# Performance work log

Hardware: AMD Instinct MI355X
Metric: run time of the kernel (lower is better)

The kernel has to match this reference:

```python
import jax, jax.numpy as jnp
import numpy as np
import math

N, E, D, H = 50000, 1600000, 128, 8
DH = D // H  # per-head dim
EPS = 1e-5   # batchnorm eps


def _attn(q_in, k_in, v_in, Wq, Wk, Wv, src, dst):
    # GAT-style edge attention: score = exp(clip(<K[src],Q[dst]>/sqrt(DH), -5, 5))
    Q = (q_in @ Wq.T).reshape(-1, H, DH)
    K = (k_in @ Wk.T).reshape(-1, H, DH)
    V = (v_in @ Wv.T).reshape(-1, H, DH)
    score = jnp.exp(jnp.clip((K[src] * Q[dst]).sum(-1) / math.sqrt(DH), -5.0, 5.0))  # [E,H]
    wV = jax.ops.segment_sum(V[src] * score[:, :, None], dst, num_segments=N)  # [N,H,DH]
    z = jax.ops.segment_sum(score, dst, num_segments=N)                         # [N,H]
    return (wV / z[:, :, None]).reshape(-1, D)


def _bn(x, gamma, beta):
    # BatchNorm1d in training mode: biased batch stats over nodes
    m = x.mean(0)
    v = x.var(0)
    return (x - m) / jnp.sqrt(v + EPS) * gamma + beta


def setup_inputs() -> dict:
    key = jax.random.key(0)
    ks = iter(jax.random.split(key, 48))

    def w(shape, scale=None):
        s = scale if scale is not None else 1.0 / math.sqrt(shape[-1])
        return jax.random.normal(next(ks), shape, jnp.float32) * s

    inp = dict(
        h=w((N, D), 1.0),
        sv=w((N, D), 1.0),
        src=jax.random.randint(next(ks), (E,), 0, N, jnp.int32),
        dst=jax.random.randint(next(ks), (E,), 0, N, jnp.int32),
    )
    for nm in ["Wq_sv", "Wk_sv", "Wv_sv", "Wq_cv", "Wk_cv", "Wv_cv",
               "Wq_sh", "Wk_sh", "Wv_sh"]:
        inp[nm] = w((D, D))
    inp.update(
        Wo=w((D, 2 * D)), bo=jnp.zeros((D,), jnp.float32),
        Wo_h=w((D, 2 * D)), bo_h=jnp.zeros((D,), jnp.float32),
        W1=w((2 * D, D)), b1=jnp.zeros((2 * D,), jnp.float32),
        W2=w((D, 2 * D)), b2=jnp.zeros((D,), jnp.float32),
        W1h=w((2 * D, D)), b1h=jnp.zeros((2 * D,), jnp.float32),
        W2h=w((D, 2 * D)), b2h=jnp.zeros((D,), jnp.float32),
        Wg1=w((D, D)), bg1=jnp.zeros((D,), jnp.float32),
        Wg2=w((D, D)), bg2=jnp.zeros((D,), jnp.float32),
        gbn1=jnp.ones((D,), jnp.float32), bbn1=jnp.zeros((D,), jnp.float32),
        gbn2=jnp.ones((D,), jnp.float32), bbn2=jnp.zeros((D,), jnp.float32),
        gbn1h=jnp.ones((D,), jnp.float32), bbn1h=jnp.zeros((D,), jnp.float32),
        gbn2h=jnp.ones((D,), jnp.float32), bbn2h=jnp.zeros((D,), jnp.float32),
    )
    return inp


def reference(h, sv, src, dst,
              Wq_sv, Wk_sv, Wv_sv, Wq_cv, Wk_cv, Wv_cv, Wq_sh, Wk_sh, Wv_sh,
              Wo, bo, Wo_h, bo_h,
              W1, b1, W2, b2, W1h, b1h, W2h, b2h,
              Wg1, bg1, Wg2, bg2,
              gbn1, bbn1, gbn2, bbn2, gbn1h, bbn1h, gbn2h, bbn2h):
    h_in1, sv_in1 = h, sv
    # --- h branch ---
    a_self = _attn(h, h, h, Wq_sv, Wk_sv, Wv_sv, src, dst)
    a_cross = _attn(h, sv, sv, Wq_cv, Wk_cv, Wv_cv, src, dst)
    hO = jnp.concatenate([a_self, a_cross], -1) @ Wo.T + bo
    h1 = _bn(h_in1 + hO, gbn1, bbn1)
    ffn = jax.nn.relu(h1 @ W1.T + b1) @ W2.T + b2
    h_out = _bn(h1 + ffn, gbn2, bbn2)
    # --- state-vector branch ---
    a_self_h = _attn(sv, sv, sv, Wq_sh, Wk_sh, Wv_sh, src, dst)
    # faithful to source: cross_attention_v weights reused here
    a_cross_h = _attn(sv, h_in1, h_in1, Wq_cv, Wk_cv, Wv_cv, src, dst)
    svO = jnp.concatenate([a_self_h, a_cross_h], -1) @ Wo_h.T + bo_h
    g1 = jax.nn.sigmoid(h_in1 @ Wg1.T + bg1)
    sv1 = _bn((1.0 - g1) * sv_in1 + g1 * svO, gbn1h, bbn1h)
    ffn_h = jax.nn.relu(sv1 @ W1h.T + b1h) @ W2h.T + b2h
    g2 = jax.nn.sigmoid(h_in1 @ Wg2.T + bg2)
    sv_out = _bn((1.0 - g2) * sv1 + g2 * ffn_h, gbn2h, bbn2h)
    return (h_out, sv_out)
```

## Files before the change

### kernel.cpp

```cpp
#include <hip/hip_runtime.h>

typedef _Float16 f16x8 __attribute__((ext_vector_type(8)));
typedef _Float16 f16x2 __attribute__((ext_vector_type(2)));
typedef __fp16 fp16x2_raw __attribute__((ext_vector_type(2)));
typedef float f32x4 __attribute__((ext_vector_type(4)));
typedef float f32x2 __attribute__((ext_vector_type(2)));
typedef unsigned int uint32;
typedef unsigned short ushort16;
typedef unsigned char uchar;

#define EPS_BN 1e-5f

__device__ __forceinline__ uint32 pk16(float a, float b){
  fp16x2_raw h = __builtin_amdgcn_cvt_pkrtz(a, b);
  return *(uint32*)&h;
}
__device__ __forceinline__ uchar f2fp8(float f){
  uint32 p = __builtin_amdgcn_cvt_pk_fp8_f32(f, f, 0, false);
  return (uchar)(p & 0xff);
}
__device__ __forceinline__ f32x2 fp8pair_lo(uint32 w){
  return __builtin_amdgcn_cvt_pk_f32_fp8(w, false);
}
__device__ __forceinline__ f32x2 fp8pair_hi(uint32 w){
  return __builtin_amdgcn_cvt_pk_f32_fp8(w, true);
}

struct WEnt { const float* s; const float* s2; ushort16* d; int KD, MD, nfrag; };
struct WConv { WEnt e[16]; };

__global__ __launch_bounds__(256) void prep_k(WConv wc,
    const float* __restrict__ a, const float* __restrict__ b,
    ushort16* __restrict__ da, ushort16* __restrict__ db, int n,
    const int* __restrict__ dst, int* __restrict__ bcnt, int E, int shift){
  int y = blockIdx.y;
  if (y < 2){
    const float* s = y ? b : a;
    ushort16* d = y ? db : da;
    int i = (blockIdx.x * 256 + threadIdx.x) * 4;
    if (i >= n) return;
    float4 v = *(const float4*)(s + i);
    uint2 p;
    p.x = pk16(v.x, v.y);
    p.y = pk16(v.z, v.w);
    *(uint2*)(d + i) = p;
  } else if (y == 2){
    __shared__ int lh[128];
    if (blockIdx.x >= 512) return;
    int tid = threadIdx.x;
    if (tid < 128) lh[tid] = 0;
    __syncthreads();
    int stride = 512 * 256;
    for (int i = blockIdx.x * 256 + tid; i < E; i += stride)
      atomicAdd(&lh[dst[i] >> shift], 1);
    __syncthreads();
    if (tid < 128 && lh[tid]) atomicAdd(&bcnt[tid], lh[tid]);
  } else {
    if (blockIdx.x >= 256) return;
    WEnt t = wc.e[blockIdx.x >> 4];
    int fid = (blockIdx.x & 15) * 256 + threadIdx.x;
    if (fid >= t.nfrag) return;
    int lane = fid & 63, sm = fid >> 6;
    int MT = t.MD >> 4;
    int s = sm / MT, m = sm - s * MT;
    int row = m * 16 + (lane & 15);
    int col = s * 32 + (lane >> 4) * 8;
    const float* sp = t.s;
    if (t.s2 && row >= 128){ sp = t.s2; row -= 128; }
    const float* p = sp + (size_t)row * t.KD + col;
    uint4 o;
    o.x = pk16(p[0], p[1]); o.y = pk16(p[2], p[3]);
    o.z = pk16(p[4], p[5]); o.w = pk16(p[6], p[7]);
    *(uint4*)(t.d + (size_t)fid * 8) = o;
  }
}

__global__ __launch_bounds__(64) void bscan_k(const int* __restrict__ bcnt,
    int* __restrict__ bstart, int* __restrict__ bcur, int B){
  if (threadIdx.x == 0){
    int run = 0;
    for (int b = 0; b < B; b++){ bstart[b] = run; bcur[b] = run; run += bcnt[b]; }
    bstart[B] = run;
  }
}

#define BIN_TB 512
#define BIN_TILE 4096
__global__ __launch_bounds__(512) void bin_k(const int* __restrict__ src, const int* __restrict__ dst,
                                             int* __restrict__ bcur, uint2* __restrict__ ebuf,
                                             int E, int shift, int B){
  __shared__ int lhist[128];
  __shared__ int lstart[128];
  __shared__ int gbase[128];
  __shared__ uint2 lpair[BIN_TILE];
  int tid = threadIdx.x;
  int base = blockIdx.x * BIN_TILE;
  int cnt = E - base; if (cnt > BIN_TILE) cnt = BIN_TILE;
  if (tid < 128) lhist[tid] = 0;
  __syncthreads();
  int myb[8], myrank[8];
  uint2 myp[8];
  int nmine = 0;
  #pragma unroll
  for (int j = 0; j < 8; j++){
    int i = tid + j * BIN_TB;
    if (i < cnt){
      int s = src[base + i], d = dst[base + i];
      int b = d >> shift;
      myp[nmine] = make_uint2((uint32)s, (uint32)d);
      myb[nmine] = b;
      myrank[nmine] = atomicAdd(&lhist[b], 1);
      nmine++;
    }
  }
  __syncthreads();
  if (tid == 0){
    int run = 0;
    for (int b = 0; b < B; b++){ lstart[b] = run; run += lhist[b]; }
  }
  __syncthreads();
  if (tid < B) gbase[tid] = atomicAdd(&bcur[tid], lhist[tid]);
  for (int j = 0; j < nmine; j++){
    lpair[lstart[myb[j]] + myrank[j]] = myp[j];
  }
  __syncthreads();
  for (int i = tid; i < cnt; i += BIN_TB){
    uint2 p = lpair[i];
    int b = (int)(p.y >> shift);
    ebuf[gbase[b] + (i - lstart[b])] = p;
  }
}

#define CSR_TB 1024
__global__ __launch_bounds__(1024) void csr_k(const uint2* __restrict__ ebuf,
    const int* __restrict__ bstart, int* __restrict__ row_off, int* __restrict__ esrc,
    int shift, int N, int E, int B){
  __shared__ int lc[4096];
  __shared__ int lcur[4096];
  __shared__ int wsum[16];
  int b = blockIdx.x;
  int d0 = b << shift;
  int nd = 1 << shift; if (d0 + nd > N) nd = N - d0;
  if (nd <= 0) return;
  int e0 = bstart[b], e1 = bstart[b + 1];
  int tid = threadIdx.x, lane = tid & 63, wv = tid >> 6;
  for (int j = tid; j < nd; j += CSR_TB){ lc[j] = 0; lcur[j] = 0; }
  __syncthreads();
  for (int i = e0 + tid; i < e1; i += CSR_TB){
    atomicAdd(&lc[(int)ebuf[i].y - d0], 1);
  }
  __syncthreads();
  int base4 = tid * 4;
  int v0 = (base4 + 0 < nd) ? lc[base4 + 0] : 0;
  int v1 = (base4 + 1 < nd) ? lc[base4 + 1] : 0;
  int v2 = (base4 + 2 < nd) ? lc[base4 + 2] : 0;
  int v3 = (base4 + 3 < nd) ? lc[base4 + 3] : 0;
  int ts = v0 + v1 + v2 + v3;
  int inc = ts;
  #pragma unroll
  for (int d = 1; d < 64; d <<= 1){
    int t = __shfl_up(inc, d);
    if (lane >= d) inc += t;
  }
  if (lane == 63) wsum[wv] = inc;
  __syncthreads();
  int woff = 0;
  for (int w = 0; w < 16; w++) if (w < wv) woff += wsum[w];
  int excl = woff + (inc - ts);
  int o0 = excl, o1 = o0 + v0, o2 = o1 + v1, o3 = o2 + v2;
  __syncthreads();
  if (base4 + 0 < nd){ lc[base4 + 0] = o0; row_off[d0 + base4 + 0] = e0 + o0; }
  if (base4 + 1 < nd){ lc[base4 + 1] = o1; row_off[d0 + base4 + 1] = e0 + o1; }
  if (base4 + 2 < nd){ lc[base4 + 2] = o2; row_off[d0 + base4 + 2] = e0 + o2; }
  if (base4 + 3 < nd){ lc[base4 + 3] = o3; row_off[d0 + base4 + 3] = e0 + o3; }
  __syncthreads();
  for (int i = e0 + tid; i < e1; i += CSR_TB){
    uint2 p = ebuf[i];
    int d = (int)p.y - d0;
    int r = atomicAdd(&lcur[d], 1);
    esrc[e0 + lc[d] + r] = (int)p.x;
  }
  if (b == B - 1 && tid == 0) row_off[N] = E;
}

template<int KD, int MD, int EPI, int ABN, int ST, int GS>
__device__ __forceinline__ void gemm_body(
    const ushort16* __restrict__ X, const ushort16* __restrict__ W,
    const float* __restrict__ bias, const float* __restrict__ bias2,
    const ushort16* __restrict__ resb, const ushort16* __restrict__ gatep,
    const float* __restrict__ rstats, const float* __restrict__ rg, const float* __restrict__ rb,
    const float* __restrict__ astats, const float* __restrict__ ag, const float* __restrict__ ab,
    ushort16* __restrict__ outb, float* __restrict__ stats_out, int N, float invN,
    _Float16* OsBase, float* sstB, float* sst2B)
{
  constexpr int KS = KD / 32;
  constexpr int MT = MD / 16;
  constexpr int LSTR = MD + 8;
  int lane = threadIdx.x & 63, wv = threadIdx.x >> 6;
  _Float16* OsW = OsBase + wv * 16 * LSTR;
  int l15 = lane & 15, kq = lane >> 4;
  int rowbase = (blockIdx.x * 4 + wv) * 16;
  int row = rowbase + l15;
  int rc = row < N ? row : N - 1;
  const f16x8* ap = (const f16x8*)(X + (size_t)rc * KD + kq * 8);
  f16x8 a[KS];
  #pragma unroll
  for (int s = 0; s < KS; s++) a[s] = ap[s * 4];
  if constexpr (ABN){
    #pragma unroll
    for (int s = 0; s < KS; s++){
      #pragma unroll
      for (int j = 0; j < 8; j++){
        int c = s * 32 + kq * 8 + j;
        float mm = astats[c] * invN;
        float var = astats[128 + c] * invN - mm * mm;
        float rs = rsqrtf(var + EPS_BN);
        float scc = rs * ag[c];
        float shh = ab[c] - mm * scc;
        a[s][j] = (_Float16)((float)a[s][j] * scc + shh);
      }
    }
  }
  const f16x8* Wf = (const f16x8*)W;
  f32x4 acc[MT];
  #pragma unroll
  for (int m = 0; m < MT; m++) acc[m] = (f32x4)(0.f);
  #pragma unroll
  for (int s = 0; s < KS; s++){
    #pragma unroll
    for (int m = 0; m < MT; m++){
      acc[m] = __builtin_amdgcn_mfma_f32_16x16x32_f16(a[s], Wf[(s * MT + m) * 64 + lane], acc[m], 0, 0, 0);
    }
  }
  float ps[MT], ps2[MT];
  if constexpr (ST){
    #pragma unroll
    for (int m = 0; m < MT; m++){ ps[m] = 0.f; ps2[m] = 0.f; }
  }
  int r0 = rowbase + kq * 4;
  #pragma unroll
  for (int m = 0; m < MT; m++){
    int col = m * 16 + l15;
    float bv;
    if (bias2 && col >= 128) bv = bias2[col - 128];
    else bv = bias[col];
    float sc = 0.f, sh = 0.f;
    if constexpr (EPI == 5 || EPI == 6){
      float mm = rstats[col] * invN;
      float var = rstats[128 + col] * invN - mm * mm;
      float rs = rsqrtf(var + EPS_BN);
      sc = rs * rg[col]; sh = rb[col] - mm * sc;
    }
    #pragma unroll
    for (int r = 0; r < 4; r++){
      int rr = r0 + r;
      float v;
      {
        int rrc = rr < N ? rr : N - 1;
        v = acc[m][r] + bv;
        if constexpr (EPI == 1) v = fmaxf(v, 0.f);
        if constexpr (EPI == 2) v = 1.f / (1.f + __expf(-v));
        if constexpr (EPI == 3){
          union { ushort16 u; _Float16 h; } cv; cv.u = resb[(size_t)rrc * 128 + col];
          v += (float)cv.h;
        }
        if constexpr (EPI == 5){
          union { ushort16 u; _Float16 h; } cv; cv.u = resb[(size_t)rrc * 128 + col];
          v += (float)cv.h * sc + sh;
        }
        if constexpr (EPI == 4 || EPI == 6){
          union { ushort16 u; _Float16 h; } gv; gv.u = gatep[(size_t)rrc * GS + col];
          union { ushort16 u; _Float16 h; } cv; cv.u = resb[(size_t)rrc * 128 + col];
          float g = (float)gv.h;
          float rv = (float)cv.h;
          if constexpr (EPI == 6) rv = rv * sc + sh;
          v = (1.f - g) * rv + g * v;
        }
      }
      OsW[(kq * 4 + r) * LSTR + col] = (_Float16)v;
      if constexpr (ST){
        if (rr < N){ ps[m] += v; ps2[m] += v * v; }
      }
    }
  }
  if constexpr (MD == 128){
    #pragma unroll
    for (int p = 0; p < 4; p++){
      int lrow = p * 4 + (lane >> 4);
      int rr = rowbase + lrow;
      int col8 = l15 * 8;
      if (rr < N){
        uint4 ov = *(uint4*)&OsW[lrow * LSTR + col8];
        *(uint4*)(outb + (size_t)rr * MD + col8) = ov;
      }
    }
  } else {
    #pragma unroll
    for (int p = 0; p < 8; p++){
      int lrow = p * 2 + (lane >> 5);
      int rr = rowbase + lrow;
      int col8 = (lane & 31) * 8;
      if (rr < N){
        uint4 ov = *(uint4*)&OsW[lrow * LSTR + col8];
        *(uint4*)(outb + (size_t)rr * MD + col8) = ov;
      }
    }
  }
  if constexpr (ST){
    #pragma unroll
    for (int m = 0; m < MT; m++){
      float s = ps[m], s2 = ps2[m];
      s  += __shfl_xor(s, 16);  s  += __shfl_xor(s, 32);
      s2 += __shfl_xor(s2, 16); s2 += __shfl_xor(s2, 32);
      if (lane < 16){ sstB[wv * 128 + m * 16 + l15] = s; sst2B[wv * 128 + m * 16 + l15] = s2; }
    }
    __syncthreads();
    int tid = threadIdx.x;
    if (tid < 128){
      atomicAdd(&stats_out[tid], sstB[tid] + sstB[128 + tid] + sstB[256 + tid] + sstB[384 + tid]);
    } else {
      int c = tid - 128;
      atomicAdd(&stats_out[tid], sst2B[c] + sst2B[128 + c] + sst2B[256 + c] + sst2B[384 + c]);
    }
  }
}

struct QkvArgs {
  const ushort16* Xq[4];
  const ushort16* Xkv[4];
  const ushort16* Wq[4];
  const ushort16* Wk[4];
  const ushort16* Wv[4];
  ushort16* Qo[4];
};
__global__ __launch_bounds__(256) void qkvg_k(
    QkvArgs A, uchar* __restrict__ KV8,
    const ushort16* __restrict__ Xg, const ushort16* __restrict__ Wg,
    const float* __restrict__ bg1, const float* __restrict__ bg2,
    ushort16* __restrict__ Gout, int N, float invN)
{
  __shared__ char smem[38144];
  int slot = blockIdx.y;
  if (slot == 4){
    _Float16* Os = (_Float16*)smem;
    float* sst  = (float*)(smem + 33792);
    float* sst2 = (float*)(smem + 33792 + 2048);
    gemm_body<128,256,2,0,0,256>(Xg, Wg, bg1, bg2, nullptr, nullptr,
        nullptr, nullptr, nullptr, nullptr, nullptr, nullptr,
        Gout, nullptr, N, invN, Os, sst, sst2);
    return;
  }
  _Float16* Qs = (_Float16*)smem;
  uchar* Ks = (uchar*)(smem + 17408);
  uchar* Vs = (uchar*)(smem + 17408 + 8704);
  int toff = slot << 8;
  const ushort16* Xq = A.Xq[slot];
  const ushort16* Xkv = A.Xkv[slot];
  ushort16* Qo = A.Qo[slot];
  int lane = threadIdx.x & 63, wv = threadIdx.x >> 6;
  _Float16* QsW = Qs + wv * 16 * 136;
  uchar* KsW = Ks + wv * 16 * 136;
  uchar* VsW = Vs + wv * 16 * 136;
  int l15 = lane & 15, kq = lane >> 4;
  int rowbase = (blockIdx.x * 4 + wv) * 16;
  int row = rowbase + l15;
  int rc = row < N ? row : N - 1;
  const f16x8* aq = (const f16x8*)(Xq + (size_t)rc * 128 + kq * 8);
  const f16x8* ak = (const f16x8*)(Xkv + (size_t)rc * 128 + kq * 8);
  f16x8 Aq[4], Ak[4];
  #pragma unroll
  for (int s = 0; s < 4; s++){ Aq[s] = aq[s * 4]; Ak[s] = ak[s * 4]; }
  const f16x8* Wqf = (const f16x8*)A.Wq[slot];
  const f16x8* Wkf = (const f16x8*)A.Wk[slot];
  const f16x8* Wvf = (const f16x8*)A.Wv[slot];
  f32x4 q[8], k[8], v[8];
  #pragma unroll
  for (int m = 0; m < 8; m++){ q[m] = (f32x4)(0.f); k[m] = (f32x4)(0.f); v[m] = (f32x4)(0.f); }
  #pragma unroll
  for (int s = 0; s < 4; s++){
    #pragma unroll
    for (int m = 0; m < 8; m++){
      int fi = (s * 8 + m) * 64 + lane;
      q[m] = __builtin_amdgcn_mfma_f32_16x16x32_f16(Aq[s], Wqf[fi], q[m], 0, 0, 0);
      k[m] = __builtin_amdgcn_mfma_f32_16x16x32_f16(Ak[s], Wkf[fi], k[m], 0, 0, 0);
      v[m] = __builtin_amdgcn_mfma_f32_16x16x32_f16(Ak[s], Wvf[fi], v[m], 0, 0, 0);
    }
  }
  #pragma unroll
  for (int m = 0; m < 8; m++){
    int col = m * 16 + l15;
    #pragma unroll
    for (int r = 0; r < 4; r++){
      int lrow = kq * 4 + r;
      QsW[lrow * 136 + col] = (_Float16)q[m][r];
      KsW[lrow * 136 + col] = f2fp8(k[m][r]);
      VsW[lrow * 136 + col] = f2fp8(v[m][r]);
    }
  }
  #pragma unroll
  for (int p = 0; p < 4; p++){
    int lrow = p * 4 + (lane >> 4);
    int rr = rowbase + lrow;
    int col8 = l15 * 8;
    if (rr < N){
      uint4 qv = *(uint4*)&QsW[lrow * 136 + col8];
      *(uint4*)(Qo + (size_t)rr * 128 + col8) = qv;
      uint2 kv = *(uint2*)&KsW[lrow * 136 + col8];
      *(uint2*)(KV8 + (size_t)rr * 1024 + toff + col8) = kv;
      uint2 vv = *(uint2*)&VsW[lrow * 136 + col8];
      *(uint2*)(KV8 + (size_t)rr * 1024 + toff + 128 + col8) = vv;
    }
  }
}

struct GPairArgs {
  const ushort16* X[2]; const ushort16* W[2];
  const float* bias[2];
  const ushort16* resb[2]; const ushort16* gatep[2];
  const float* rstats[2]; const float* rg[2]; const float* rb[2];
  const float* astats[2]; const float* ag[2]; const float* ab[2];
  ushort16* outb[2]; float* stats_out[2];
};
template<int KD, int MD, int EPI0, int EPI1, int ABN, int ST, int GS>
__global__ __launch_bounds__(256) void gemm_pair_k(GPairArgs A, int N, float invN)
{
  __shared__ _Float16 Os[4 * 16 * (MD + 8)];
  __shared__ float sst[512];
  __shared__ float sst2[512];
  int y = blockIdx.y;
  if (y == 0){
    gemm_body<KD, MD, EPI0, ABN, ST, GS>(A.X[0], A.W[0], A.bias[0], nullptr, A.resb[0], A.gatep[0],
        A.rstats[0], A.rg[0], A.rb[0], A.astats[0], A.ag[0], A.ab[0],
        A.outb[0], A.stats_out[0], N, invN, Os, sst, sst2);
  } else {
    gemm_body<KD, MD, EPI1, ABN, ST, GS>(A.X[1], A.W[1], A.bias[1], nullptr, A.resb[1], A.gatep[1],
        A.rstats[1], A.rg[1], A.rb[1], A.astats[1], A.ag[1], A.ab[1],
        A.outb[1], A.stats_out[1], N, invN, Os, sst, sst2);
  }
}

__global__ __launch_bounds__(256) void attn4_k(
    const ushort16* __restrict__ Qa, const ushort16* __restrict__ Qb,
    const ushort16* __restrict__ Qc, const ushort16* __restrict__ Qd,
    const uchar* __restrict__ KV,
    const int* __restrict__ row_off, const int* __restrict__ esrc,
    ushort16* __restrict__ cat_h, ushort16* __restrict__ cat_sv, int n0, int n1)
{
  int wv = threadIdx.x >> 6, lane = threadIdx.x & 63;
  int n = n0 + blockIdx.x * 4 + wv;
  if (n >= n1) return;
  int g = lane >> 4, j = lane & 15;
  uint32 j8 = (uint32)j * 8u;
  const float QS = 0.25f * 1.44269504088896f;
  const float CL = 7.21347520444482f;
  const ushort16* Qp[4] = {Qa, Qb, Qc, Qd};
  f32x2 q[4][4];
  #pragma unroll
  for (int t = 0; t < 4; t++){
    uint4 u = *(const uint4*)(Qp[t] + (size_t)n * 128 + j8);
    f16x2 h0 = *(f16x2*)&u.x, h1 = *(f16x2*)&u.y;
    f16x2 h2 = *(f16x2*)&u.z, h3 = *(f16x2*)&u.w;
    q[t][0].x = (float)h0.x * QS; q[t][0].y = (float)h0.y * QS;
    q[t][1].x = (float)h1.x * QS; q[t][1].y = (float)h1.y * QS;
    q[t][2].x = (float)h2.x * QS; q[t][2].y = (float)h2.y * QS;
    q[t][3].x = (float)h3.x * QS; q[t][3].y = (float)h3.y * QS;
  }
  int e0 = row_off[n], e1 = row_off[n + 1];
  int itmax = (e1 - e0 + 3) >> 2;
  f32x2 ac[4][4];
  #pragma unroll
  for (int t = 0; t < 4; t++){
    #pragma unroll
    for (int r = 0; r < 4; r++) ac[t][r] = (f32x2)(0.f);
  }
  float z[4] = {0.f, 0.f, 0.f, 0.f};
  int e = e0 + g;
  int s = (e < e1) ? esrc[e] : -1;
  uint32 off = ((uint32)(s < 0 ? 0 : s) << 10) + j8;
  uint2 kc[4], vc[4];
  #pragma unroll
  for (int t = 0; t < 4; t++){
    kc[t] = *(const uint2*)(KV + off + t * 256);
    vc[t] = *(const uint2*)(KV + off + t * 256 + 128);
  }
  for (int it = 0; it < itmax; ++it){
    int e2 = e + 4;
    int s2 = (e2 < e1) ? esrc[e2] : -1;
    uint32 off2 = ((uint32)(s2 < 0 ? 0 : s2) << 10) + j8;
    uint2 kn[4], vn[4];
    #pragma unroll
    for (int t = 0; t < 4; t++){
      kn[t] = *(const uint2*)(KV + off2 + t * 256);
      vn[t] = *(const uint2*)(KV + off2 + t * 256 + 128);
    }
    if (s >= 0){
      #pragma unroll
      for (int t = 0; t < 4; t++){
        f32x2 k0 = fp8pair_lo(kc[t].x), k1 = fp8pair_hi(kc[t].x);
        f32x2 k2 = fp8pair_lo(kc[t].y), k3 = fp8pair_hi(kc[t].y);
        f32x2 dd = k0 * q[t][0] + k1 * q[t][1] + k2 * q[t][2] + k3 * q[t][3];
        float d = dd.x + dd.y;
        d += __shfl_xor(d, 1);
        float sc = __builtin_amdgcn_exp2f(__builtin_amdgcn_fmed3f(d, -CL, CL));
        f32x2 v0 = fp8pair_lo(vc[t].x), v1 = fp8pair_hi(vc[t].x);
        f32x2 v2 = fp8pair_lo(vc[t].y), v3 = fp8pair_hi(vc[t].y);
        f32x2 sv; sv.x = sc; sv.y = sc;
        ac[t][0] += sv * v0; ac[t][1] += sv * v1;
        ac[t][2] += sv * v2; ac[t][3] += sv * v3;
        z[t] += sc;
      }
    }
    e = e2; s = s2; off = off2;
    #pragma unroll
    for (int t = 0; t < 4; t++){ kc[t] = kn[t]; vc[t] = vn[t]; }
  }
  #pragma unroll
  for (int t = 0; t < 4; t++){
    #pragma unroll
    for (int r = 0; r < 4; r++){
      ac[t][r].x += __shfl_xor(ac[t][r].x, 16);
      ac[t][r].y += __shfl_xor(ac[t][r].y, 16);
      ac[t][r].x += __shfl_xor(ac[t][r].x, 32);
      ac[t][r].y += __shfl_xor(ac[t][r].y, 32);
    }
    z[t] += __shfl_xor(z[t], 16);
    z[t] += __shfl_xor(z[t], 32);
  }
  if (g == 0){
    size_t base = (size_t)n * 256 + j8;
    #pragma unroll
    for (int t = 0; t < 4; t++){
      float rz = __builtin_amdgcn_rcpf(z[t]);
      uint4 o;
      o.x = pk16(ac[t][0].x * rz, ac[t][0].y * rz);
      o.y = pk16(ac[t][1].x * rz, ac[t][1].y * rz);
      o.z = pk16(ac[t][2].x * rz, ac[t][2].y * rz);
      o.w = pk16(ac[t][3].x * rz, ac[t][3].y * rz);
      ushort16* dp = (t < 2) ? cat_h : cat_sv;
      *(uint4*)(dp + base + (t & 1) * 128) = o;
    }
  }
}

struct Bn2Args {
  const ushort16* x[2]; const float* stats[2];
  const float* g[2]; const float* b[2]; float* out[2];
};
__global__ __launch_bounds__(256) void bn2_k(Bn2Args A, int total4, float invN)
{
  int y = blockIdx.y;
  int i = blockIdx.x * 256 + threadIdx.x;
  if (i >= total4) return;
  const ushort16* x = A.x[y];
  const float* stats = A.stats[y];
  const float* gamma = A.g[y];
  const float* beta = A.b[y];
  float* outf = A.out[y];
  uint2 xp = *(const uint2*)(x + (size_t)i * 4);
  f16x2 x01 = *(f16x2*)&xp.x, x23 = *(f16x2*)&xp.y;
  float xv[4] = {(float)x01.x, (float)x01.y, (float)x23.x, (float)x23.y};
  int c0 = (i * 4) & 127;
  float o[4];
  #pragma unroll
  for (int j = 0; j < 4; j++){
    int c = c0 + j;
    float m = stats[c] * invN;
    float var = stats[128 + c] * invN - m * m;
    float rstd = rsqrtf(var + EPS_BN);
    o[j] = (xv[j] - m) * rstd * gamma[c] + beta[c];
  }
  *(float4*)(outf + (size_t)i * 4) = make_float4(o[0], o[1], o[2], o[3]);
}

extern "C" void kernel_launch(void* const* d_in, const int* in_sizes, int n_in,
                              void* d_out, int out_size, void* d_ws, size_t ws_size,
                              hipStream_t stream) {
  const float* h   = (const float*)d_in[0];
  const float* sv  = (const float*)d_in[1];
  const int* src   = (const int*)d_in[2];
  const int* dst   = (const int*)d_in[3];
  const int N = in_sizes[0] / 128;
  const int E = in_sizes[2];

  char* wsb = (char*)d_ws;
  size_t o = 0;
  auto take = [&](size_t bytes)->size_t{
    size_t r = o;
    o = (o + bytes + 255) & ~(size_t)255;
    return r;
  };
  size_t big = (size_t)E * 8;
  if (big < (size_t)N * 1024) big = (size_t)N * 1024;
  size_t bcnt_off   = take(128 * 4);
  size_t stats_off  = take(4 * 256 * 4);
  size_t bstart_off = take(132 * 4);
  size_t bcur_off   = take(128 * 4);
  size_t rowoff_off = take((size_t)(N + 1) * 4);
  size_t esrc_off   = take((size_t)E * 4);
  size_t big_off    = take(big);
  size_t wpool_off  = take((size_t)376832 * 2);
  size_t hf_off     = take((size_t)N * 128 * 2);
  size_t svf_off    = take((size_t)N * 128 * 2);
  size_t cath_off   = take((size_t)N * 256 * 2);
  size_t catsv_off  = take((size_t)N * 256 * 2);
  size_t Q1_off     = take((size_t)N * 128 * 2);
  size_t Q2_off     = take((size_t)N * 128 * 2);
  size_t X1_off     = take((size_t)N * 128 * 2);
  size_t X2_off     = take((size_t)N * 128 * 2);
  size_t G_off      = take((size_t)N * 256 * 2);

  int*    bcnt    = (int*)(wsb + bcnt_off);
  float*  stats   = (float*)(wsb + stats_off);
  int*    bstart  = (int*)(wsb + bstart_off);
  int*    bcur    = (int*)(wsb + bcur_off);
  int*    row_off = (int*)(wsb + rowoff_off);
  int*    esrc    = (int*)(wsb + esrc_off);
  uint2*  ebuf    = (uint2*)(wsb + big_off);
  uchar*  KVall   = (uchar*)(wsb + big_off);
  ushort16* wpool = (ushort16*)(wsb + wpool_off);
  ushort16* h_f   = (ushort16*)(wsb + hf_off);
  ushort16* sv_f  = (ushort16*)(wsb + svf_off);
  ushort16* cat_h = (ushort16*)(wsb + cath_off);
  ushort16* cat_sv= (ushort16*)(wsb + catsv_off);
  ushort16* Q1    = (ushort16*)(wsb + Q1_off);
  ushort16* Q2    = (ushort16*)(wsb + Q2_off);
  ushort16* Xb1   = (ushort16*)(wsb + X1_off);
  ushort16* Xb2   = (ushort16*)(wsb + X2_off);
  ushort16* Gbuf  = (ushort16*)(wsb + G_off);
  ushort16* Q3 = Xb1;
  ushort16* Q4 = Xb2;

  ushort16* Wq_sv = wpool + 0 * 16384;
  ushort16* Wk_sv = wpool + 1 * 16384;
  ushort16* Wv_sv = wpool + 2 * 16384;
  ushort16* Wq_cv = wpool + 3 * 16384;
  ushort16* Wk_cv = wpool + 4 * 16384;
  ushort16* Wv_cv = wpool + 5 * 16384;
  ushort16* Wq_sh = wpool + 6 * 16384;
  ushort16* Wk_sh = wpool + 7 * 16384;
  ushort16* Wv_sh = wpool + 8 * 16384;
  ushort16* Wgb   = wpool + 147456;
  ushort16* Wob   = wpool + 180224;
  ushort16* Wohb  = wpool + 212992;
  ushort16* W1b   = wpool + 245760;
  ushort16* W2b   = wpool + 278528;
  ushort16* W1hb  = wpool + 311296;
  ushort16* W2hb  = wpool + 344064;

  const float* bo   = (const float*)d_in[14];
  const float* bo_h = (const float*)d_in[16];
  const float* b1   = (const float*)d_in[18];
  const float* b2   = (const float*)d_in[20];
  const float* b1h  = (const float*)d_in[22];
  const float* b2h  = (const float*)d_in[24];
  const float* bg1  = (const float*)d_in[26];
  const float* bg2  = (const float*)d_in[28];
  const float* gbn1  = (const float*)d_in[29];
  const float* bbn1  = (const float*)d_in[30];
  const float* gbn2  = (const float*)d_in[31];
  const float* bbn2  = (const float*)d_in[32];
  const float* gbn1h = (const float*)d_in[33];
  const float* bbn1h = (const float*)d_in[34];
  const float* gbn2h = (const float*)d_in[35];
  const float* bbn2h = (const float*)d_in[36];

  float* out_h  = (float*)d_out;
  float* out_sv = out_h + (size_t)N * 128;

  (void)hipMemsetAsync(wsb, 0, stats_off + 4 * 256 * 4, stream);

  WConv wc;
  {
    auto set = [&](int i, int din, int din2, size_t dstoff, int KD, int MD){
      wc.e[i].s  = (const float*)d_in[din];
      wc.e[i].s2 = (din2 >= 0) ? (const float*)d_in[din2] : nullptr;
      wc.e[i].d  = wpool + dstoff;
      wc.e[i].KD = KD; wc.e[i].MD = MD;
      wc.e[i].nfrag = KD * MD / 8;
    };
    for (int i = 0; i < 9; i++) set(i, 4 + i, -1, (size_t)i * 16384, 128, 128);
    set(9,  25, 27, 147456, 128, 256);
    set(10, 13, -1, 180224, 256, 128);
    set(11, 15, -1, 212992, 256, 128);
    set(12, 17, -1, 245760, 128, 256);
    set(13, 19, -1, 278528, 256, 128);
    set(14, 21, -1, 311296, 128, 256);
    set(15, 23, -1, 344064, 256, 128);
  }

  int shift = 9;
  while ((((N - 1) >> shift) + 1) > 128) shift++;
  const int B = ((N - 1) >> shift) + 1;

  int nelem = N * 128;
  int CVB = (nelem / 4 + 255) / 256;
  int PXB = CVB > 512 ? CVB : 512;
  prep_k<<<dim3(PXB, 4), 256, 0, stream>>>(wc, h, sv, h_f, sv_f, nelem, dst, bcnt, E, shift);

  bscan_k<<<1, 64, 0, stream>>>(bcnt, bstart, bcur, B);
  bin_k<<<(E + BIN_TILE - 1) / BIN_TILE, BIN_TB, 0, stream>>>(src, dst, bcur, ebuf, E, shift, B);
  csr_k<<<B, CSR_TB, 0, stream>>>(ebuf, bstart, row_off, esrc, shift, N, E, B);

  const int GB = (N + 63) / 64;
  const int T4 = nelem / 4;
  const int APB = (T4 + 255) / 256;
  const float invN = 1.f / (float)N;

  QkvArgs qa;
  qa.Xq[0] = h_f;  qa.Xkv[0] = h_f;  qa.Wq[0] = Wq_sv; qa.Wk[0] = Wk_sv; qa.Wv[0] = Wv_sv; qa.Qo[0] = Q1;
  qa.Xq[1] = h_f;  qa.Xkv[1] = sv_f; qa.Wq[1] = Wq_cv; qa.Wk[1] = Wk_cv; qa.Wv[1] = Wv_cv; qa.Qo[1] = Q2;
  qa.Xq[2] = sv_f; qa.Xkv[2] = sv_f; qa.Wq[2] = Wq_sh; qa.Wk[2] = Wk_sh; qa.Wv[2] = Wv_sh; qa.Qo[2] = Q3;
  qa.Xq[3] = sv_f; qa.Xkv[3] = h_f;  qa.Wq[3] = Wq_cv; qa.Wk[3] = Wk_cv; qa.Wv[3] = Wv_cv; qa.Qo[3] = Q4;
  qkvg_k<<<dim3(GB, 5), 256, 0, stream>>>(qa, KVall, h_f, Wgb, bg1, bg2, Gbuf, N, invN);

  {
    int per = ((N + 5) / 6 + 3) & ~3;
    for (int n0 = 0; n0 < N; n0 += per){
      int n1 = n0 + per; if (n1 > N) n1 = N;
      attn4_k<<<(n1 - n0 + 3) / 4, 256, 0, stream>>>(Q1, Q2, Q3, Q4, KVall,
                                                     row_off, esrc, cat_h, cat_sv, n0, n1);
    }
  }

  {
    GPairArgs A = {};
    A.X[0] = cat_h;  A.W[0] = Wob;  A.bias[0] = bo;   A.resb[0] = h_f;  A.gatep[0] = nullptr;
    A.outb[0] = Xb1; A.stats_out[0] = stats;
    A.X[1] = cat_sv; A.W[1] = Wohb; A.bias[1] = bo_h; A.resb[1] = sv_f; A.gatep[1] = Gbuf;
    A.outb[1] = Q1;  A.stats_out[1] = stats + 512;
    gemm_pair_k<256,128,3,4,0,1,256><<<dim3(GB, 2), 256, 0, stream>>>(A, N, invN);
  }
  {
    GPairArgs A = {};
    A.X[0] = Xb1; A.W[0] = W1b;  A.bias[0] = b1;
    A.astats[0] = stats;       A.ag[0] = gbn1;  A.ab[0] = bbn1;  A.outb[0] = cat_h;
    A.X[1] = Q1;  A.W[1] = W1hb; A.bias[1] = b1h;
    A.astats[1] = stats + 512; A.ag[1] = gbn1h; A.ab[1] = bbn1h; A.outb[1] = cat_sv;
    gemm_pair_k<128,256,1,1,1,0,256><<<dim3(GB, 2), 256, 0, stream>>>(A, N, invN);
  }
  {
    GPairArgs A = {};
    A.X[0] = cat_h;  A.W[0] = W2b;  A.bias[0] = b2;  A.resb[0] = Xb1;
    A.rstats[0] = stats;       A.rg[0] = gbn1;  A.rb[0] = bbn1;
    A.outb[0] = Xb2; A.stats_out[0] = stats + 256;
    A.X[1] = cat_sv; A.W[1] = W2hb; A.bias[1] = b2h; A.resb[1] = Q1;  A.gatep[1] = Gbuf + 128;
    A.rstats[1] = stats + 512; A.rg[1] = gbn1h; A.rb[1] = bbn1h;
    A.outb[1] = Q2;  A.stats_out[1] = stats + 768;
    gemm_pair_k<256,128,5,6,0,1,256><<<dim3(GB, 2), 256, 0, stream>>>(A, N, invN);
  }
  {
    Bn2Args A;
    A.x[0] = Xb2; A.stats[0] = stats + 256; A.g[0] = gbn2;  A.b[0] = bbn2;  A.out[0] = out_h;
    A.x[1] = Q2;  A.stats[1] = stats + 768; A.g[1] = gbn2h; A.b[1] = bbn2h; A.out[1] = out_sv;
    bn2_k<<<dim3(APB, 2), 256, 0, stream>>>(A, T4, invN);
  }
}
```

Before: 783.2 us.

## Split gate GEMM out, serialize QKV projections, launch attention once

```diff
diff --git a/kernel.cpp b/kernel.cpp
--- a/kernel.cpp
+++ b/kernel.cpp
@@ -325,6 +325,22 @@
   }
 }
 
+template<int KD, int MD, int EPI, int ABN, int ST, int GS>
+__global__ __launch_bounds__(256) void gemm_k(
+    const ushort16* __restrict__ X, const ushort16* __restrict__ W,
+    const float* __restrict__ bias, const float* __restrict__ bias2,
+    const ushort16* __restrict__ resb, const ushort16* __restrict__ gatep,
+    const float* __restrict__ rstats, const float* __restrict__ rg, const float* __restrict__ rb,
+    const float* __restrict__ astats, const float* __restrict__ ag, const float* __restrict__ ab,
+    ushort16* __restrict__ outb, float* __restrict__ stats_out, int N, float invN)
+{
+  __shared__ _Float16 Os[4 * 16 * (MD + 8)];
+  __shared__ float sst[512];
+  __shared__ float sst2[512];
+  gemm_body<KD, MD, EPI, ABN, ST, GS>(X, W, bias, bias2, resb, gatep, rstats, rg, rb,
+                                      astats, ag, ab, outb, stats_out, N, invN, Os, sst, sst2);
+}
+
 struct QkvArgs {
   const ushort16* Xq[4];
   const ushort16* Xkv[4];
@@ -333,34 +349,17 @@
   const ushort16* Wv[4];
   ushort16* Qo[4];
 };
-__global__ __launch_bounds__(256) void qkvg_k(
-    QkvArgs A, uchar* __restrict__ KV8,
-    const ushort16* __restrict__ Xg, const ushort16* __restrict__ Wg,
-    const float* __restrict__ bg1, const float* __restrict__ bg2,
-    ushort16* __restrict__ Gout, int N, float invN)
+__global__ __launch_bounds__(256) void qkv_k(QkvArgs A, uchar* __restrict__ KV8, int N)
 {
-  __shared__ char smem[38144];
+  __shared__ _Float16 S[4][16 * 136];
   int slot = blockIdx.y;
-  if (slot == 4){
-    _Float16* Os = (_Float16*)smem;
-    float* sst  = (float*)(smem + 33792);
-    float* sst2 = (float*)(smem + 33792 + 2048);
-    gemm_body<128,256,2,0,0,256>(Xg, Wg, bg1, bg2, nullptr, nullptr,
-        nullptr, nullptr, nullptr, nullptr, nullptr, nullptr,
-        Gout, nullptr, N, invN, Os, sst, sst2);
-    return;
-  }
-  _Float16* Qs = (_Float16*)smem;
-  uchar* Ks = (uchar*)(smem + 17408);
-  uchar* Vs = (uchar*)(smem + 17408 + 8704);
   int toff = slot << 8;
   const ushort16* Xq = A.Xq[slot];
   const ushort16* Xkv = A.Xkv[slot];
   ushort16* Qo = A.Qo[slot];
   int lane = threadIdx.x & 63, wv = threadIdx.x >> 6;
-  _Float16* QsW = Qs + wv * 16 * 136;
-  uchar* KsW = Ks + wv * 16 * 136;
-  uchar* VsW = Vs + wv * 16 * 136;
+  _Float16* SW = S[wv];
+  uchar* SB = (uchar*)SW;
   int l15 = lane & 15, kq = lane >> 4;
   int rowbase = (blockIdx.x * 4 + wv) * 16;
   int row = rowbase + l15;
@@ -373,41 +372,85 @@
   const f16x8* Wqf = (const f16x8*)A.Wq[slot];
   const f16x8* Wkf = (const f16x8*)A.Wk[slot];
   const f16x8* Wvf = (const f16x8*)A.Wv[slot];
-  f32x4 q[8], k[8], v[8];
-  #pragma unroll
-  for (int m = 0; m < 8; m++){ q[m] = (f32x4)(0.f); k[m] = (f32x4)(0.f); v[m] = (f32x4)(0.f); }
+  f32x4 acc[8];
+
+  #pragma unroll
+  for (int m = 0; m < 8; m++) acc[m] = (f32x4)(0.f);
   #pragma unroll
   for (int s = 0; s < 4; s++){
     #pragma unroll
     for (int m = 0; m < 8; m++){
-      int fi = (s * 8 + m) * 64 + lane;
-      q[m] = __builtin_amdgcn_mfma_f32_16x16x32_f16(Aq[s], Wqf[fi], q[m], 0, 0, 0);
-      k[m] = __builtin_amdgcn_mfma_f32_16x16x32_f16(Ak[s], Wkf[fi], k[m], 0, 0, 0);
-      v[m] = __builtin_amdgcn_mfma_f32_16x16x32_f16(Ak[s], Wvf[fi], v[m], 0, 0, 0);
+      acc[m] = __builtin_amdgcn_mfma_f32_16x16x32_f16(Aq[s], Wqf[(s * 8 + m) * 64 + lane], acc[m], 0, 0, 0);
     }
   }
   #pragma unroll
   for (int m = 0; m < 8; m++){
     int col = m * 16 + l15;
     #pragma unroll
-    for (int r = 0; r < 4; r++){
-      int lrow = kq * 4 + r;
-      QsW[lrow * 136 + col] = (_Float16)q[m][r];
-      KsW[lrow * 136 + col] = f2fp8(k[m][r]);
-      VsW[lrow * 136 + col] = f2fp8(v[m][r]);
-    }
+    for (int r = 0; r < 4; r++)
+      SW[(kq * 4 + r) * 136 + col] = (_Float16)acc[m][r];
   }
   #pragma unroll
   for (int p = 0; p < 4; p++){
-    int lrow = p * 4 + (lane >> 4);
+    int lrow = p * 4 + kq;
     int rr = rowbase + lrow;
     int col8 = l15 * 8;
     if (rr < N){
-      uint4 qv = *(uint4*)&QsW[lrow * 136 + col8];
+      uint4 qv = *(uint4*)&SW[lrow * 136 + col8];
       *(uint4*)(Qo + (size_t)rr * 128 + col8) = qv;
-      uint2 kv = *(uint2*)&KsW[lrow * 136 + col8];
+    }
+  }
+
+  #pragma unroll
+  for (int m = 0; m < 8; m++) acc[m] = (f32x4)(0.f);
+  #pragma unroll
+  for (int s = 0; s < 4; s++){
+    #pragma unroll
+    for (int m = 0; m < 8; m++){
+      acc[m] = __builtin_amdgcn_mfma_f32_16x16x32_f16(Ak[s], Wkf[(s * 8 + m) * 64 + lane], acc[m], 0, 0, 0);
+    }
+  }
+  #pragma unroll
+  for (int m = 0; m < 8; m++){
+    int col = m * 16 + l15;
+    #pragma unroll
+    for (int r = 0; r < 4; r++)
+      SB[(kq * 4 + r) * 136 + col] = f2fp8(acc[m][r]);
+  }
+  #pragma unroll
+  for (int p = 0; p < 4; p++){
+    int lrow = p * 4 + kq;
+    int rr = rowbase + lrow;
+    int col8 = l15 * 8;
+    if (rr < N){
+      uint2 kv = *(uint2*)&SB[lrow * 136 + col8];
       *(uint2*)(KV8 + (size_t)rr * 1024 + toff + col8) = kv;
-      uint2 vv = *(uint2*)&VsW[lrow * 136 + col8];
+    }
+  }
+
+  #pragma unroll
+  for (int m = 0; m < 8; m++) acc[m] = (f32x4)(0.f);
+  #pragma unroll
+  for (int s = 0; s < 4; s++){
+    #pragma unroll
+    for (int m = 0; m < 8; m++){
+      acc[m] = __builtin_amdgcn_mfma_f32_16x16x32_f16(Ak[s], Wvf[(s * 8 + m) * 64 + lane], acc[m], 0, 0, 0);
+    }
+  }
+  #pragma unroll
+  for (int m = 0; m < 8; m++){
+    int col = m * 16 + l15;
+    #pragma unroll
+    for (int r = 0; r < 4; r++)
+      SB[(kq * 4 + r) * 136 + col] = f2fp8(acc[m][r]);
+  }
+  #pragma unroll
+  for (int p = 0; p < 4; p++){
+    int lrow = p * 4 + kq;
+    int rr = rowbase + lrow;
+    int col8 = l15 * 8;
+    if (rr < N){
+      uint2 vv = *(uint2*)&SB[lrow * 136 + col8];
       *(uint2*)(KV8 + (size_t)rr * 1024 + toff + 128 + col8) = vv;
     }
   }
@@ -702,25 +745,21 @@
   csr_k<<<B, CSR_TB, 0, stream>>>(ebuf, bstart, row_off, esrc, shift, N, E, B);
 
   const int GB = (N + 63) / 64;
+  const int AB = (N + 3) / 4;
   const int T4 = nelem / 4;
   const int APB = (T4 + 255) / 256;
   const float invN = 1.f / (float)N;
+
+  gemm_k<128,256,2,0,0,256><<<GB, 256, 0, stream>>>(h_f, Wgb, bg1, bg2, nullptr, nullptr,
+      nullptr, nullptr, nullptr, nullptr, nullptr, nullptr, Gbuf, nullptr, N, invN);
 
   QkvArgs qa;
   qa.Xq[0] = h_f;  qa.Xkv[0] = h_f;  qa.Wq[0] = Wq_sv; qa.Wk[0] = Wk_sv; qa.Wv[0] = Wv_sv; qa.Qo[0] = Q1;
   qa.Xq[1] = h_f;  qa.Xkv[1] = sv_f; qa.Wq[1] = Wq_cv; qa.Wk[1] = Wk_cv; qa.Wv[1] = Wv_cv; qa.Qo[1] = Q2;
   qa.Xq[2] = sv_f; qa.Xkv[2] = sv_f; qa.Wq[2] = Wq_sh; qa.Wk[2] = Wk_sh; qa.Wv[2] = Wv_sh; qa.Qo[2] = Q3;
   qa.Xq[3] = sv_f; qa.Xkv[3] = h_f;  qa.Wq[3] = Wq_cv; qa.Wk[3] = Wk_cv; qa.Wv[3] = Wv_cv; qa.Qo[3] = Q4;
-  qkvg_k<<<dim3(GB, 5), 256, 0, stream>>>(qa, KVall, h_f, Wgb, bg1, bg2, Gbuf, N, invN);
-
-  {
-    int per = ((N + 5) / 6 + 3) & ~3;
-    for (int n0 = 0; n0 < N; n0 += per){
-      int n1 = n0 + per; if (n1 > N) n1 = N;
-      attn4_k<<<(n1 - n0 + 3) / 4, 256, 0, stream>>>(Q1, Q2, Q3, Q4, KVall,
-                                                     row_off, esrc, cat_h, cat_sv, n0, n1);
-    }
-  }
+  qkv_k<<<dim3(GB, 4), 256, 0, stream>>>(qa, KVall, N);
+  attn4_k<<<AB, 256, 0, stream>>>(Q1, Q2, Q3, Q4, KVall, row_off, esrc, cat_h, cat_sv, 0, N);
 
   {
     GPairArgs A = {};
```

Result: faster. 722.9 us (-7.7%).
